# Kernel tuning notes

Hardware: AMD Instinct MI355X
Metric: run time of the kernel (lower is better)

The kernel has to match this reference:

```python
import jax, jax.numpy as jnp
import numpy as np

B, N, D = 8, 4096, 3

def setup_inputs() -> dict:
    key = jax.random.key(0)
    k1, k2 = jax.random.split(key)
    prediction = jax.random.normal(k1, (B, N, D), dtype=jnp.float32)
    ground_truth = jax.random.normal(k2, (B, N, D), dtype=jnp.float32)
    return {"prediction": prediction, "ground_truth": ground_truth}

def reference(prediction, ground_truth):
    batch_size, num, _ = prediction.shape
    # T[b, i, j] = ||pred[b, i] - gt[b, j]||^2  -> [B, N, N]
    diff = prediction[:, :, None, :] - ground_truth[:, None, :, :]
    T = jnp.sum(diff * diff, axis=-1)
    # squeeze() in torch is a no-op for B > 1
    cd_loss = jnp.sum(jnp.min(T, axis=1)) + jnp.sum(jnp.min(T, axis=2))
    return cd_loss / batch_size
```

## Files before the change

### kernel.cpp

```cpp
#include <hip/hip_runtime.h>

#define TPB 256
#define IPT 8
#define NIB 2
#define NPTS 4096
#define NB 8

__global__ __launch_bounds__(TPB, 6) void cd_partial_kernel(
    const float* __restrict__ pred, const float* __restrict__ gt,
    float* __restrict__ partial, float* __restrict__ out, int njb, int jchunk) {
  extern __shared__ float4 sg[];

  if (blockIdx.x == 0 && threadIdx.x == 0) *out = 0.0f;

  int bid = blockIdx.x;
  int jb  = bid % njb;  bid /= njb;
  int ib  = bid & (NIB - 1); bid /= NIB;
  int b   = bid & (NB - 1);  bid /= NB;
  int dir = bid;

  const float* src = (dir == 0) ? pred : gt;
  const float* tgt = (dir == 0) ? gt : pred;
  src += (size_t)b * NPTS * 3;
  tgt += (size_t)b * NPTS * 3;

  const int t = threadIdx.x;

  for (int p = t; p < jchunk; p += TPB) {
    int j = jb * jchunk + p;
    float gx = tgt[j * 3 + 0];
    float gy = tgt[j * 3 + 1];
    float gz = tgt[j * 3 + 2];
    sg[p] = make_float4(gx, gy, gz, fmaf(gx, gx, fmaf(gy, gy, gz * gz)));
  }

  const int ibase = ib * (TPB * IPT);
  const float4* sv = (const float4*)(src + (size_t)(ibase + t * IPT) * 3);
  float4 A = sv[0], B2 = sv[1], C = sv[2], D = sv[3], E = sv[4], F = sv[5];
  float x[IPT], y[IPT], z[IPT];
  x[0]=A.x;  y[0]=A.y;  z[0]=A.z;
  x[1]=A.w;  y[1]=B2.x; z[1]=B2.y;
  x[2]=B2.z; y[2]=B2.w; z[2]=C.x;
  x[3]=C.y;  y[3]=C.z;  z[3]=C.w;
  x[4]=D.x;  y[4]=D.y;  z[4]=D.z;
  x[5]=D.w;  y[5]=E.x;  z[5]=E.y;
  x[6]=E.z;  y[6]=E.w;  z[6]=F.x;
  x[7]=F.y;  y[7]=F.z;  z[7]=F.w;

  float qx[IPT], qy[IPT], qz[IPT], pp[IPT], mn[IPT];
#pragma unroll
  for (int k = 0; k < IPT; ++k) {
    qx[k] = -2.0f * x[k];
    qy[k] = -2.0f * y[k];
    qz[k] = -2.0f * z[k];
    pp[k] = fmaf(x[k], x[k], fmaf(y[k], y[k], z[k] * z[k]));
    mn[k] = 3.4e38f;
  }
  __syncthreads();

#pragma unroll 4
  for (int p = 0; p < jchunk; p += 2) {
    float4 g0 = sg[p];
    float4 g1 = sg[p + 1];
#pragma unroll
    for (int k = 0; k < IPT; ++k) {
      float v0 = fmaf(qx[k], g0.x, fmaf(qy[k], g0.y, fmaf(qz[k], g0.z, g0.w)));
      float v1 = fmaf(qx[k], g1.x, fmaf(qy[k], g1.y, fmaf(qz[k], g1.z, g1.w)));
      mn[k] = fminf(mn[k], fminf(v0, v1));
    }
  }

  float* outp = partial + ((size_t)((dir * NB + b) * njb + jb)) * NPTS + ibase + t * IPT;
  float4 s0 = make_float4(mn[0] + pp[0], mn[1] + pp[1], mn[2] + pp[2], mn[3] + pp[3]);
  float4 s1 = make_float4(mn[4] + pp[4], mn[5] + pp[5], mn[6] + pp[6], mn[7] + pp[7]);
  ((float4*)outp)[0] = s0;
  ((float4*)outp)[1] = s1;
}

__global__ __launch_bounds__(TPB) void cd_reduce_kernel(
    const float* __restrict__ partial, float* __restrict__ out, int njb) {
  const int total = 2 * NB * NPTS;
  int tid = blockIdx.x * TPB + threadIdx.x;
  float local = 0.0f;
  for (int s = tid; s < total; s += gridDim.x * TPB) {
    int db = s >> 12;
    int i  = s & (NPTS - 1);
    const float* p = partial + (size_t)db * njb * NPTS + i;
    float m = p[0];
#pragma unroll 8
    for (int jb = 1; jb < njb; ++jb) m = fminf(m, p[(size_t)jb * NPTS]);
    local += m;
  }
#pragma unroll
  for (int off = 32; off > 0; off >>= 1) local += __shfl_down(local, off, 64);
  __shared__ float red[TPB / 64];
  int wave = threadIdx.x >> 6;
  int lane = threadIdx.x & 63;
  if (lane == 0) red[wave] = local;
  __syncthreads();
  if (threadIdx.x == 0) {
    float s = 0.0f;
    for (int w = 0; w < TPB / 64; ++w) s += red[w];
    atomicAdd(out, s * (1.0f / NB));
  }
}

extern "C" void kernel_launch(void* const* d_in, const int* in_sizes, int n_in,
                              void* d_out, int out_size, void* d_ws, size_t ws_size,
                              hipStream_t stream) {
  const float* pred = (const float*)d_in[0];
  const float* gt   = (const float*)d_in[1];
  float* out        = (float*)d_out;
  float* partial    = (float*)d_ws;

  int njb = 64;
  {
    size_t per_jb = (size_t)2 * NB * NPTS * sizeof(float);
    size_t need = per_jb * njb;
    if (ws_size < need) {
      njb = (int)(ws_size / per_jb);
      if (njb < 1) njb = 1;
      while (njb & (njb - 1)) njb &= njb - 1;
      if (njb > 64) njb = 64;
    }
  }
  int jchunk = NPTS / njb;

  dim3 grid(2 * NB * NIB * njb);
  size_t lds = (size_t)jchunk * sizeof(float4);
  cd_partial_kernel<<<grid, TPB, lds, stream>>>(pred, gt, partial, out, njb, jchunk);
  cd_reduce_kernel<<<256, TPB, 0, stream>>>(partial, out, njb);
}
```

Baseline: 45.95 us.

## Use packed v_pk_fma_f32 with SoA-paired LDS layout and fewer j-blocks

The target points are stored in LDS as interleaved pairs (x0,x1,y0,y1,z0,z1,w0,w1), so each point's distance to two targets is computed with three packed v_pk_fma_f32 instructions instead of six scalar FMAs. The aim is to halve FMA issue count in the inner loop. The j-split drops from 64 to 32 blocks, which shrinks the partial buffer and the reduce work but gives each block a longer loop and half as many blocks. Launch bounds drop to 4 waves to allow more registers for the duplicated packed operands.

```diff
diff --git a/kernel.cpp b/kernel.cpp
--- a/kernel.cpp
+++ b/kernel.cpp
@@ -6,10 +6,18 @@
 #define NPTS 4096
 #define NB 8
 
-__global__ __launch_bounds__(TPB, 6) void cd_partial_kernel(
+typedef float v2f __attribute__((ext_vector_type(2)));
+
+static __device__ __forceinline__ v2f pk_fma(v2f a, v2f b, v2f c) {
+  v2f d;
+  asm("v_pk_fma_f32 %0, %1, %2, %3" : "=v"(d) : "v"(a), "v"(b), "v"(c));
+  return d;
+}
+
+__global__ __launch_bounds__(TPB, 4) void cd_partial_kernel(
     const float* __restrict__ pred, const float* __restrict__ gt,
     float* __restrict__ partial, float* __restrict__ out, int njb, int jchunk) {
-  extern __shared__ float4 sg[];
+  extern __shared__ float4 spr[];
 
   if (blockIdx.x == 0 && threadIdx.x == 0) *out = 0.0f;
 
@@ -26,12 +34,18 @@
 
   const int t = threadIdx.x;
 
-  for (int p = t; p < jchunk; p += TPB) {
-    int j = jb * jchunk + p;
-    float gx = tgt[j * 3 + 0];
-    float gy = tgt[j * 3 + 1];
-    float gz = tgt[j * 3 + 2];
-    sg[p] = make_float4(gx, gy, gz, fmaf(gx, gx, fmaf(gy, gy, gz * gz)));
+  for (int j = t; j < jchunk; j += TPB) {
+    int jj = jb * jchunk + j;
+    float gx = tgt[jj * 3 + 0];
+    float gy = tgt[jj * 3 + 1];
+    float gz = tgt[jj * 3 + 2];
+    float gw = fmaf(gx, gx, fmaf(gy, gy, gz * gz));
+    int p = j >> 1, h = j & 1;
+    float* base = (float*)&spr[2 * p];
+    base[0 + h] = gx;
+    base[2 + h] = gy;
+    base[4 + h] = gz;
+    base[6 + h] = gw;
   }
 
   const int ibase = ib * (TPB * IPT);
@@ -47,26 +61,34 @@
   x[6]=E.z;  y[6]=E.w;  z[6]=F.x;
   x[7]=F.y;  y[7]=F.z;  z[7]=F.w;
 
-  float qx[IPT], qy[IPT], qz[IPT], pp[IPT], mn[IPT];
+  v2f qx2[IPT], qy2[IPT], qz2[IPT];
+  float pp[IPT], mn[IPT];
 #pragma unroll
   for (int k = 0; k < IPT; ++k) {
-    qx[k] = -2.0f * x[k];
-    qy[k] = -2.0f * y[k];
-    qz[k] = -2.0f * z[k];
+    float qx = -2.0f * x[k], qy = -2.0f * y[k], qz = -2.0f * z[k];
+    qx2[k] = (v2f){qx, qx};
+    qy2[k] = (v2f){qy, qy};
+    qz2[k] = (v2f){qz, qz};
     pp[k] = fmaf(x[k], x[k], fmaf(y[k], y[k], z[k] * z[k]));
     mn[k] = 3.4e38f;
   }
   __syncthreads();
 
-#pragma unroll 4
-  for (int p = 0; p < jchunk; p += 2) {
-    float4 g0 = sg[p];
-    float4 g1 = sg[p + 1];
+  const int npair = jchunk >> 1;
+#pragma unroll 8
+  for (int p = 0; p < npair; ++p) {
+    float4 u = spr[2 * p];
+    float4 w = spr[2 * p + 1];
+    v2f X = (v2f){u.x, u.y};
+    v2f Y = (v2f){u.z, u.w};
+    v2f Z = (v2f){w.x, w.y};
+    v2f W = (v2f){w.z, w.w};
 #pragma unroll
     for (int k = 0; k < IPT; ++k) {
-      float v0 = fmaf(qx[k], g0.x, fmaf(qy[k], g0.y, fmaf(qz[k], g0.z, g0.w)));
-      float v1 = fmaf(qx[k], g1.x, fmaf(qy[k], g1.y, fmaf(qz[k], g1.z, g1.w)));
-      mn[k] = fminf(mn[k], fminf(v0, v1));
+      v2f acc = pk_fma(qz2[k], Z, W);
+      acc = pk_fma(qy2[k], Y, acc);
+      acc = pk_fma(qx2[k], X, acc);
+      mn[k] = fminf(mn[k], fminf(acc.x, acc.y));
     }
   }
 
@@ -113,7 +135,7 @@
   float* out        = (float*)d_out;
   float* partial    = (float*)d_ws;
 
-  int njb = 64;
+  int njb = 32;
   {
     size_t per_jb = (size_t)2 * NB * NPTS * sizeof(float);
     size_t need = per_jb * njb;
@@ -121,7 +143,7 @@
       njb = (int)(ws_size / per_jb);
       if (njb < 1) njb = 1;
       while (njb & (njb - 1)) njb &= njb - 1;
-      if (njb > 64) njb = 64;
+      if (njb > 32) njb = 32;
     }
   }
   int jchunk = NPTS / njb;
```

After: 39.49 us. -14.0%, faster.
